# Optimization experiments

Hardware: AMD Instinct MI355X
Metric: run time of the kernel (lower is better)

## Reference

```python
import jax, jax.numpy as jnp
import numpy as np

N_NODES = 100000
N_EDGES = 600000
D = 128          # embedding_dim == hidden_dim
OUT = 128        # output_dim
L = 5            # number of GINConv layers


def setup_inputs() -> dict:
    key = jax.random.key(0)
    ks = jax.random.split(key, 9)
    return {
        "x": jax.random.randint(ks[0], (N_NODES,), 0, N_NODES),
        "edge_index": jax.random.randint(ks[1], (2, N_EDGES), 0, N_NODES),
        "emb": jax.random.normal(ks[2], (N_NODES, D), dtype=jnp.float32) * 0.02,
        "Wa": jax.random.normal(ks[3], (L, D, D), dtype=jnp.float32) * 0.05,
        "ba": jnp.zeros((L, D), dtype=jnp.float32),
        "Wb": jax.random.normal(ks[4], (L, D, D), dtype=jnp.float32) * 0.05,
        "bb": jnp.zeros((L, D), dtype=jnp.float32),
        "Wlin": jax.random.normal(ks[5], (D, OUT), dtype=jnp.float32) * 0.05,
        "blin": jnp.zeros((OUT,), dtype=jnp.float32),
    }


def reference(x, edge_index, emb, Wa, ba, Wb, bb, Wlin, blin):
    src, dst = edge_index[0], edge_index[1]
    h = emb[x]  # [N, D] embedding lookup
    for l in range(L):
        # GINConv with eps=0: mlp((1+eps)*x_i + sum_{j->i} x_j)
        agg = jax.ops.segment_sum(h[src], dst, num_segments=N_NODES)  # [N, D]
        z = h + agg
        z = jax.nn.relu(z @ Wa[l] + ba[l])  # MLP hidden
        z = z @ Wb[l] + bb[l]               # MLP out
        h = jax.nn.relu(z)                  # outer F.relu in forward
    pooled = jnp.sum(h, axis=0, keepdims=True)  # global_add_pool, batch=None -> [1, D]
    return pooled @ Wlin + blin                  # [1, OUT]
```

## Files before the change

### kernel.cpp

```cpp
#include <hip/hip_runtime.h>

#define D 128
#define NLAYERS 5

using short8  = __attribute__((ext_vector_type(8))) short;
using short4v = __attribute__((ext_vector_type(4))) short;
using floatx4 = __attribute__((ext_vector_type(4))) float;
using floatx2 = __attribute__((ext_vector_type(2))) float;

__device__ __forceinline__ unsigned bf16_rne(float x) {
    unsigned u = __float_as_uint(x);
    return (u + 0x7fffu + ((u >> 16) & 1u)) >> 16;
}
__device__ __forceinline__ float bf16_to_f32(short s) {
    return __uint_as_float(((unsigned)(unsigned short)s) << 16);
}

#define HSCALE 16.0f
#define HSCALE_INV 0.0625f

__global__ void prepA_kernel(const int* __restrict__ x, const float* __restrict__ emb,
                             const float* __restrict__ Wa, const float* __restrict__ Wb,
                             const int* __restrict__ edst,
                             unsigned char* __restrict__ H0, short* __restrict__ wt,
                             int* __restrict__ deg,
                             int n_nodes, int n_edges) {
    const int gtid = blockIdx.x * 256 + threadIdx.x;
    const int gsz  = gridDim.x * 256;
    for (int g = gtid; g < 2 * NLAYERS * D * D; g += gsz) {
        int mat = g >> 14, idx = g & 16383;
        int n = idx >> 7, k = idx & 127;
        const float* W = (mat & 1) ? (Wb + (size_t)(mat >> 1) * D * D)
                                   : (Wa + (size_t)(mat >> 1) * D * D);
        wt[g] = (short)bf16_rne(W[k * D + n]);
    }
    for (int t = gtid; t < n_nodes * 32; t += gsz) {
        int node = t >> 5, lane = t & 31;
        int s = x[node];
        const float4 v = *reinterpret_cast<const float4*>(emb + (size_t)s * D + lane * 4);
        int w = __builtin_amdgcn_cvt_pk_fp8_f32(v.x * HSCALE, v.y * HSCALE, 0, false);
        w = __builtin_amdgcn_cvt_pk_fp8_f32(v.z * HSCALE, v.w * HSCALE, w, true);
        reinterpret_cast<unsigned int*>(H0)[(size_t)node * 32 + lane] = (unsigned int)w;
    }
    for (int e = gtid; e < n_edges; e += gsz) atomicAdd(&deg[edst[e]], 1);
}

#define SCAN_TILE 1024
__global__ void scan_sums_kernel(const int* __restrict__ deg, int* __restrict__ bsums, int n) {
    __shared__ int red[256];
    int base = blockIdx.x * SCAN_TILE + threadIdx.x * 4;
    int s = 0;
    #pragma unroll
    for (int j = 0; j < 4; j++) {
        int i = base + j;
        if (i < n) s += deg[i];
    }
    red[threadIdx.x] = s;
    __syncthreads();
    for (int off = 128; off > 0; off >>= 1) {
        if (threadIdx.x < off) red[threadIdx.x] += red[threadIdx.x + off];
        __syncthreads();
    }
    if (threadIdx.x == 0) bsums[blockIdx.x] = red[0];
}

__global__ void scan_bsums_kernel(int* __restrict__ bsums, int nblocks) {
    __shared__ int sdata[256];
    int carry = 0;
    for (int base = 0; base < nblocks; base += 256) {
        int i = base + threadIdx.x;
        int v = (i < nblocks) ? bsums[i] : 0;
        sdata[threadIdx.x] = v;
        __syncthreads();
        for (int off = 1; off < 256; off <<= 1) {
            int t = (threadIdx.x >= off) ? sdata[threadIdx.x - off] : 0;
            __syncthreads();
            sdata[threadIdx.x] += t;
            __syncthreads();
        }
        int incl = sdata[threadIdx.x];
        if (i < nblocks) bsums[i] = carry + incl - v;
        carry += sdata[255];
        __syncthreads();
    }
}

__global__ void scan_final_kernel(const int* __restrict__ deg, const int* __restrict__ bsums,
                                  int* __restrict__ offsets, int* __restrict__ cursor, int n) {
    __shared__ int sdata[256];
    int base = blockIdx.x * SCAN_TILE + threadIdx.x * 4;
    int v[4];
    int s = 0;
    #pragma unroll
    for (int j = 0; j < 4; j++) {
        int i = base + j;
        v[j] = (i < n) ? deg[i] : 0;
        s += v[j];
    }
    sdata[threadIdx.x] = s;
    __syncthreads();
    for (int off = 1; off < 256; off <<= 1) {
        int t = (threadIdx.x >= off) ? sdata[threadIdx.x - off] : 0;
        __syncthreads();
        sdata[threadIdx.x] += t;
        __syncthreads();
    }
    int excl = sdata[threadIdx.x] - s + bsums[blockIdx.x];
    #pragma unroll
    for (int j = 0; j < 4; j++) {
        int i = base + j;
        if (i <= n) offsets[i] = excl;
        if (i < n) cursor[i] = excl;
        excl += v[j];
    }
}

__global__ void fill_kernel(const int* __restrict__ esrc, const int* __restrict__ edst,
                            int* __restrict__ cursor, int* __restrict__ csr_src, int n_edges) {
    int e = blockIdx.x * 256 + threadIdx.x;
    if (e >= n_edges) return;
    int pos = atomicAdd(&cursor[edst[e]], 1);
    csr_src[pos] = esrc[e];
}

__global__ __launch_bounds__(256) void agg_kernel(
        const int* __restrict__ offsets, const int* __restrict__ csr_src,
        const unsigned char* __restrict__ h_in, short* __restrict__ z, int n_rows) {
    const int t   = blockIdx.x * 256 + threadIdx.x;
    const int row = t >> 3;
    const int l8  = t & 7;
    if (row >= n_rows) return;

    float acc[16];
    {
        uint4 w = *reinterpret_cast<const uint4*>(h_in + (size_t)row * D + l8 * 16);
        unsigned int wd[4] = {w.x, w.y, w.z, w.w};
        #pragma unroll
        for (int k = 0; k < 4; k++) {
            floatx2 lo = __builtin_amdgcn_cvt_pk_f32_fp8((int)wd[k], false);
            floatx2 hi = __builtin_amdgcn_cvt_pk_f32_fp8((int)wd[k], true);
            acc[4 * k]     = lo[0]; acc[4 * k + 1] = lo[1];
            acc[4 * k + 2] = hi[0]; acc[4 * k + 3] = hi[1];
        }
    }
    int e   = offsets[row];
    int end = offsets[row + 1];
    for (; e + 3 < end; e += 4) {
        int sA = csr_src[e];
        int sB = csr_src[e + 1];
        int sC = csr_src[e + 2];
        int sD = csr_src[e + 3];
        uint4 wA = *reinterpret_cast<const uint4*>(h_in + (size_t)sA * D + l8 * 16);
        uint4 wB = *reinterpret_cast<const uint4*>(h_in + (size_t)sB * D + l8 * 16);
        uint4 wC = *reinterpret_cast<const uint4*>(h_in + (size_t)sC * D + l8 * 16);
        uint4 wD = *reinterpret_cast<const uint4*>(h_in + (size_t)sD * D + l8 * 16);
        unsigned int da[4] = {wA.x, wA.y, wA.z, wA.w};
        unsigned int db[4] = {wB.x, wB.y, wB.z, wB.w};
        unsigned int dc[4] = {wC.x, wC.y, wC.z, wC.w};
        unsigned int dd[4] = {wD.x, wD.y, wD.z, wD.w};
        #pragma unroll
        for (int k = 0; k < 4; k++) {
            floatx2 alo = __builtin_amdgcn_cvt_pk_f32_fp8((int)da[k], false);
            floatx2 ahi = __builtin_amdgcn_cvt_pk_f32_fp8((int)da[k], true);
            floatx2 blo = __builtin_amdgcn_cvt_pk_f32_fp8((int)db[k], false);
            floatx2 bhi = __builtin_amdgcn_cvt_pk_f32_fp8((int)db[k], true);
            floatx2 clo = __builtin_amdgcn_cvt_pk_f32_fp8((int)dc[k], false);
            floatx2 chi = __builtin_amdgcn_cvt_pk_f32_fp8((int)dc[k], true);
            floatx2 dlo = __builtin_amdgcn_cvt_pk_f32_fp8((int)dd[k], false);
            floatx2 dhi = __builtin_amdgcn_cvt_pk_f32_fp8((int)dd[k], true);
            acc[4 * k]     += (alo[0] + blo[0]) + (clo[0] + dlo[0]);
            acc[4 * k + 1] += (alo[1] + blo[1]) + (clo[1] + dlo[1]);
            acc[4 * k + 2] += (ahi[0] + bhi[0]) + (chi[0] + dhi[0]);
            acc[4 * k + 3] += (ahi[1] + bhi[1]) + (chi[1] + dhi[1]);
        }
    }
    for (; e < end; e++) {
        int sA = csr_src[e];
        uint4 wA = *reinterpret_cast<const uint4*>(h_in + (size_t)sA * D + l8 * 16);
        unsigned int da[4] = {wA.x, wA.y, wA.z, wA.w};
        #pragma unroll
        for (int k = 0; k < 4; k++) {
            floatx2 alo = __builtin_amdgcn_cvt_pk_f32_fp8((int)da[k], false);
            floatx2 ahi = __builtin_amdgcn_cvt_pk_f32_fp8((int)da[k], true);
            acc[4 * k]     += alo[0];
            acc[4 * k + 1] += alo[1];
            acc[4 * k + 2] += ahi[0];
            acc[4 * k + 3] += ahi[1];
        }
    }
    short8 o0, o1;
    #pragma unroll
    for (int j = 0; j < 8; j++) {
        o0[j] = (short)bf16_rne(acc[j] * HSCALE_INV);
        o1[j] = (short)bf16_rne(acc[8 + j] * HSCALE_INV);
    }
    *reinterpret_cast<short8*>(z + (size_t)row * D + l8 * 16)     = o0;
    *reinterpret_cast<short8*>(z + (size_t)row * D + l8 * 16 + 8) = o1;
}

__global__ __launch_bounds__(256, 2) void mlp_kernel(
        const short* __restrict__ z, const short* __restrict__ wta,
        const short* __restrict__ wtb, const float* __restrict__ ba,
        const float* __restrict__ bb, unsigned char* __restrict__ h_out,
        float* __restrict__ pooled_accum, int n_rows, int n_tiles) {
    __shared__ __align__(16) short wash[128 * 128];
    __shared__ __align__(16) short wbsh[128 * 128];
    __shared__ __align__(16) short tsh[4][16 * 128];

    const int tid = threadIdx.x;

    #pragma unroll
    for (int i = 0; i < 8; i++) {
        int g = i * 256 + tid;
        int n = g >> 4, c = g & 15;
        int off = (n * 16 + (c ^ (n & 15))) * 8;
        *reinterpret_cast<short8*>(&wash[off]) =
            *reinterpret_cast<const short8*>(wta + n * D + c * 8);
        *reinterpret_cast<short8*>(&wbsh[off]) =
            *reinterpret_cast<const short8*>(wtb + n * D + c * 8);
    }
    __syncthreads();

    const int lane = tid & 63;
    const int wv   = tid >> 6;
    const int lm   = lane & 15;
    const int quad = lane >> 4;
    short* myt = &tsh[wv][0];

    float bva[8], bvb[8];
    #pragma unroll
    for (int cs = 0; cs < 8; cs++) {
        bva[cs] = ba[cs * 16 + lm];
        bvb[cs] = bb[cs * 16 + lm];
    }

    float poolsum[8];
    #pragma unroll
    for (int cs = 0; cs < 8; cs++) poolsum[cs] = 0.f;

    const int wave_id = blockIdx.x * 4 + wv;
    const int n_waves = gridDim.x * 4;

    for (int tile = wave_id; tile < n_tiles; tile += n_waves) {
        const int row0 = tile * 16;
        const int r    = row0 + lm;

        short8 av[4];
        #pragma unroll
        for (int ks = 0; ks < 4; ks++) {
            if (r < n_rows)
                av[ks] = *reinterpret_cast<const short8*>(z + (size_t)r * D + (ks * 4 + quad) * 8);
            else
                av[ks] = short8{0, 0, 0, 0, 0, 0, 0, 0};
        }

        floatx4 acc1[8];
        #pragma unroll
        for (int cs = 0; cs < 8; cs++) acc1[cs] = floatx4{0.f, 0.f, 0.f, 0.f};
        #pragma unroll
        for (int ks = 0; ks < 4; ks++) {
            const int c = ks * 4 + quad;
            #pragma unroll
            for (int cs = 0; cs < 8; cs++) {
                int nn = cs * 16 + lm;
                short8 bv = *reinterpret_cast<const short8*>(&wash[(nn * 16 + (c ^ (nn & 15))) * 8]);
                acc1[cs] = __builtin_amdgcn_mfma_f32_16x16x32_bf16(av[ks], bv, acc1[cs], 0, 0, 0);
            }
        }

        #pragma unroll
        for (int cs = 0; cs < 8; cs++) {
            int col = cs * 16 + lm;
            int cj = col >> 3, ci = col & 7;
            #pragma unroll
            for (int reg = 0; reg < 4; reg++) {
                int tr = quad * 4 + reg;
                float v = fmaxf(acc1[cs][reg] + bva[cs], 0.f);
                myt[(tr * 16 + (cj ^ tr)) * 8 + ci] = (short)bf16_rne(v);
            }
        }

        short8 av2[4];
        #pragma unroll
        for (int ks = 0; ks < 4; ks++) {
            const int c = ks * 4 + quad;
            av2[ks] = *reinterpret_cast<const short8*>(&myt[(lm * 16 + (c ^ lm)) * 8]);
        }

        floatx4 acc2[8];
        #pragma unroll
        for (int cs = 0; cs < 8; cs++) acc2[cs] = floatx4{0.f, 0.f, 0.f, 0.f};
        #pragma unroll
        for (int ks = 0; ks < 4; ks++) {
            const int c = ks * 4 + quad;
            #pragma unroll
            for (int cs = 0; cs < 8; cs++) {
                int nn = cs * 16 + lm;
                short8 bv = *reinterpret_cast<const short8*>(&wbsh[(nn * 16 + (c ^ (nn & 15))) * 8]);
                acc2[cs] = __builtin_amdgcn_mfma_f32_16x16x32_bf16(av2[ks], bv, acc2[cs], 0, 0, 0);
            }
        }

        #pragma unroll
        for (int cs = 0; cs < 8; cs++) {
            int col = cs * 16 + lm;
            #pragma unroll
            for (int reg = 0; reg < 4; reg++) {
                int rr = row0 + quad * 4 + reg;
                if (rr < n_rows) {
                    float v = fmaxf(acc2[cs][reg] + bvb[cs], 0.f);
                    if (h_out != nullptr) {
                        float sv = v * HSCALE;
                        int pw = __builtin_amdgcn_cvt_pk_fp8_f32(sv, sv, 0, false);
                        h_out[(size_t)rr * D + col] = (unsigned char)(pw & 0xff);
                    }
                    poolsum[cs] += v;
                }
            }
        }
    }

    if (pooled_accum != nullptr) {
        #pragma unroll
        for (int cs = 0; cs < 8; cs++) {
            float v = poolsum[cs];
            v += __shfl_xor(v, 16);
            v += __shfl_xor(v, 32);
            if (quad == 0) atomicAdd(&pooled_accum[cs * 16 + lm], v);
        }
    }
}

__global__ void final_kernel(const float* __restrict__ pooled, const float* __restrict__ Wlin,
                             const float* __restrict__ blin, float* __restrict__ out) {
    const int j = threadIdx.x;
    __shared__ float p[D];
    p[j] = pooled[j];
    __syncthreads();
    float s = blin[j];
    #pragma unroll 8
    for (int k = 0; k < D; k++) s += p[k] * Wlin[k * D + j];
    out[j] = s;
}

extern "C" void kernel_launch(void* const* d_in, const int* in_sizes, int n_in,
                              void* d_out, int out_size, void* d_ws, size_t ws_size,
                              hipStream_t stream) {
    const int*   x    = (const int*)d_in[0];
    const int*   ei   = (const int*)d_in[1];
    const float* emb  = (const float*)d_in[2];
    const float* Wa   = (const float*)d_in[3];
    const float* ba   = (const float*)d_in[4];
    const float* Wb   = (const float*)d_in[5];
    const float* bb   = (const float*)d_in[6];
    const float* Wlin = (const float*)d_in[7];
    const float* blin = (const float*)d_in[8];
    float* out = (float*)d_out;

    const int N = in_sizes[0];
    const int E = in_sizes[1] / 2;
    const int* esrc = ei;
    const int* edst = ei + E;

    unsigned char* H0 = (unsigned char*)d_ws;
    unsigned char* H1 = H0 + (size_t)N * D;
    short* zbuf = (short*)(H1 + (size_t)N * D);
    float* pooled = (float*)(zbuf + (size_t)N * D);
    int* deg     = (int*)(pooled + 128);
    int* offsets = deg + N;
    int* cursor  = offsets + (N + 1);
    int* bsums   = cursor + N;
    int* csr_src = bsums + 4096;
    uintptr_t wt_addr = ((uintptr_t)(csr_src + E) + 15) & ~(uintptr_t)15;
    short* wt = (short*)wt_addr;

    const int scan_blocks = (N + 1 + SCAN_TILE - 1) / SCAN_TILE;

    hipMemsetAsync(pooled, 0, (size_t)(128 + N) * sizeof(int), stream);

    prepA_kernel<<<1024, 256, 0, stream>>>(x, emb, Wa, Wb, edst, H0, wt, deg, N, E);
    scan_sums_kernel<<<scan_blocks, 256, 0, stream>>>(deg, bsums, N);
    scan_bsums_kernel<<<1, 256, 0, stream>>>(bsums, scan_blocks);
    scan_final_kernel<<<scan_blocks, 256, 0, stream>>>(deg, bsums, offsets, cursor, N);
    fill_kernel<<<(E + 255) / 256, 256, 0, stream>>>(esrc, edst, cursor, csr_src, E);

    const int agg_blocks = (N * 8 + 255) / 256;
    const int n_tiles    = (N + 15) / 16;
    unsigned char* hin = H0; unsigned char* hout = H1;
    for (int l = 0; l < NLAYERS; l++) {
        const bool last = (l == NLAYERS - 1);
        float* pacc = last ? pooled : nullptr;
        unsigned char* hdst = last ? nullptr : hout;
        agg_kernel<<<agg_blocks, 256, 0, stream>>>(offsets, csr_src, hin, zbuf, N);
        mlp_kernel<<<512, 256, 0, stream>>>(
            zbuf, wt + (size_t)(2 * l) * D * D, wt + (size_t)(2 * l + 1) * D * D,
            ba + (size_t)l * D, bb + (size_t)l * D, hdst, pacc, N, n_tiles);
        unsigned char* tmp = hin; hin = hout; hout = tmp;
    }

    final_kernel<<<1, 128, 0, stream>>>(pooled, Wlin, blin, out);
}
```

Before: 415.1 us.

## Split fused MLP into two GEMM kernels reading weights from global memory

Replaces the fused two-layer MLP kernel, which staged both weight matrices in LDS, with two separate kernels. Each kernel reads its weights directly from global/L2 into registers, and the first writes its ReLU output back over zbuf in place. The goal is to drop the large LDS footprint and per-block weight staging so occupancy can rise (launch bounds go to 4 blocks per SM, 1024 blocks). The cost is an extra round trip of the hidden activation through global memory, one more launch per layer, and weight reloads per tile from cache.

```diff
diff --git a/kernel.cpp b/kernel.cpp
--- a/kernel.cpp
+++ b/kernel.cpp
@@ -198,135 +198,148 @@
     *reinterpret_cast<short8*>(z + (size_t)row * D + l8 * 16 + 8) = o1;
 }
 
-__global__ __launch_bounds__(256, 2) void mlp_kernel(
-        const short* __restrict__ z, const short* __restrict__ wta,
-        const short* __restrict__ wtb, const float* __restrict__ ba,
-        const float* __restrict__ bb, unsigned char* __restrict__ h_out,
-        float* __restrict__ pooled_accum, int n_rows, int n_tiles) {
-    __shared__ __align__(16) short wash[128 * 128];
-    __shared__ __align__(16) short wbsh[128 * 128];
-    __shared__ __align__(16) short tsh[4][16 * 128];
-
-    const int tid = threadIdx.x;
-
-    #pragma unroll
-    for (int i = 0; i < 8; i++) {
-        int g = i * 256 + tid;
-        int n = g >> 4, c = g & 15;
-        int off = (n * 16 + (c ^ (n & 15))) * 8;
-        *reinterpret_cast<short8*>(&wash[off]) =
-            *reinterpret_cast<const short8*>(wta + n * D + c * 8);
-        *reinterpret_cast<short8*>(&wbsh[off]) =
-            *reinterpret_cast<const short8*>(wtb + n * D + c * 8);
-    }
-    __syncthreads();
-
+__global__ __launch_bounds__(256, 4) void gemm1_kernel(
+        short* __restrict__ zt, const short* __restrict__ wta,
+        const float* __restrict__ ba, int n_rows, int n_tiles) {
+    const int tid  = threadIdx.x;
     const int lane = tid & 63;
     const int wv   = tid >> 6;
     const int lm   = lane & 15;
     const int quad = lane >> 4;
-    short* myt = &tsh[wv][0];
-
-    float bva[8], bvb[8];
-    #pragma unroll
-    for (int cs = 0; cs < 8; cs++) {
-        bva[cs] = ba[cs * 16 + lm];
-        bvb[cs] = bb[cs * 16 + lm];
-    }
-
-    float poolsum[8];
-    #pragma unroll
-    for (int cs = 0; cs < 8; cs++) poolsum[cs] = 0.f;
+
+    float bva[8];
+    #pragma unroll
+    for (int j = 0; j < 8; j++) bva[j] = ba[j * 16 + lm];
 
     const int wave_id = blockIdx.x * 4 + wv;
     const int n_waves = gridDim.x * 4;
-
     for (int tile = wave_id; tile < n_tiles; tile += n_waves) {
         const int row0 = tile * 16;
         const int r    = row0 + lm;
-
         short8 av[4];
         #pragma unroll
         for (int ks = 0; ks < 4; ks++) {
             if (r < n_rows)
-                av[ks] = *reinterpret_cast<const short8*>(z + (size_t)r * D + (ks * 4 + quad) * 8);
+                av[ks] = *reinterpret_cast<const short8*>(zt + (size_t)r * D + (ks * 4 + quad) * 8);
             else
                 av[ks] = short8{0, 0, 0, 0, 0, 0, 0, 0};
         }
-
-        floatx4 acc1[8];
-        #pragma unroll
-        for (int cs = 0; cs < 8; cs++) acc1[cs] = floatx4{0.f, 0.f, 0.f, 0.f};
-        #pragma unroll
-        for (int ks = 0; ks < 4; ks++) {
-            const int c = ks * 4 + quad;
-            #pragma unroll
-            for (int cs = 0; cs < 8; cs++) {
-                int nn = cs * 16 + lm;
-                short8 bv = *reinterpret_cast<const short8*>(&wash[(nn * 16 + (c ^ (nn & 15))) * 8]);
-                acc1[cs] = __builtin_amdgcn_mfma_f32_16x16x32_bf16(av[ks], bv, acc1[cs], 0, 0, 0);
-            }
-        }
-
-        #pragma unroll
-        for (int cs = 0; cs < 8; cs++) {
-            int col = cs * 16 + lm;
-            int cj = col >> 3, ci = col & 7;
-            #pragma unroll
-            for (int reg = 0; reg < 4; reg++) {
-                int tr = quad * 4 + reg;
-                float v = fmaxf(acc1[cs][reg] + bva[cs], 0.f);
-                myt[(tr * 16 + (cj ^ tr)) * 8 + ci] = (short)bf16_rne(v);
-            }
-        }
-
-        short8 av2[4];
-        #pragma unroll
-        for (int ks = 0; ks < 4; ks++) {
-            const int c = ks * 4 + quad;
-            av2[ks] = *reinterpret_cast<const short8*>(&myt[(lm * 16 + (c ^ lm)) * 8]);
-        }
-
-        floatx4 acc2[8];
-        #pragma unroll
-        for (int cs = 0; cs < 8; cs++) acc2[cs] = floatx4{0.f, 0.f, 0.f, 0.f};
-        #pragma unroll
-        for (int ks = 0; ks < 4; ks++) {
-            const int c = ks * 4 + quad;
-            #pragma unroll
-            for (int cs = 0; cs < 8; cs++) {
-                int nn = cs * 16 + lm;
-                short8 bv = *reinterpret_cast<const short8*>(&wbsh[(nn * 16 + (c ^ (nn & 15))) * 8]);
-                acc2[cs] = __builtin_amdgcn_mfma_f32_16x16x32_bf16(av2[ks], bv, acc2[cs], 0, 0, 0);
-            }
-        }
-
-        #pragma unroll
-        for (int cs = 0; cs < 8; cs++) {
-            int col = cs * 16 + lm;
-            #pragma unroll
-            for (int reg = 0; reg < 4; reg++) {
-                int rr = row0 + quad * 4 + reg;
-                if (rr < n_rows) {
-                    float v = fmaxf(acc2[cs][reg] + bvb[cs], 0.f);
-                    if (h_out != nullptr) {
-                        float sv = v * HSCALE;
-                        int pw = __builtin_amdgcn_cvt_pk_fp8_f32(sv, sv, 0, false);
-                        h_out[(size_t)rr * D + col] = (unsigned char)(pw & 0xff);
-                    }
-                    poolsum[cs] += v;
+        const short* wp = wta;
+        asm volatile("" : "+s"(wp));
+        #pragma unroll
+        for (int h = 0; h < 2; h++) {
+            short8 bw[4][4];
+            #pragma unroll
+            for (int ks = 0; ks < 4; ks++)
+                #pragma unroll
+                for (int cs = 0; cs < 4; cs++) {
+                    int nn = h * 64 + cs * 16 + lm;
+                    bw[ks][cs] = *reinterpret_cast<const short8*>(
+                        wp + (size_t)nn * D + (ks * 4 + quad) * 8);
+                }
+            floatx4 acc[4];
+            #pragma unroll
+            for (int cs = 0; cs < 4; cs++) acc[cs] = floatx4{0.f, 0.f, 0.f, 0.f};
+            #pragma unroll
+            for (int ks = 0; ks < 4; ks++)
+                #pragma unroll
+                for (int cs = 0; cs < 4; cs++)
+                    acc[cs] = __builtin_amdgcn_mfma_f32_16x16x32_bf16(av[ks], bw[ks][cs], acc[cs], 0, 0, 0);
+            #pragma unroll
+            for (int cs = 0; cs < 4; cs++) {
+                int col = h * 64 + cs * 16 + lm;
+                float bv = bva[h * 4 + cs];
+                #pragma unroll
+                for (int reg = 0; reg < 4; reg++) {
+                    int rr = row0 + quad * 4 + reg;
+                    if (rr < n_rows)
+                        zt[(size_t)rr * D + col] = (short)bf16_rne(fmaxf(acc[cs][reg] + bv, 0.f));
                 }
             }
         }
     }
+}
+
+__global__ __launch_bounds__(256, 4) void gemm2_kernel(
+        const short* __restrict__ t, const short* __restrict__ wtb,
+        const float* __restrict__ bb, unsigned char* __restrict__ h_out,
+        float* __restrict__ pooled_accum, int n_rows, int n_tiles) {
+    const int tid  = threadIdx.x;
+    const int lane = tid & 63;
+    const int wv   = tid >> 6;
+    const int lm   = lane & 15;
+    const int quad = lane >> 4;
+
+    float bvb[8];
+    #pragma unroll
+    for (int j = 0; j < 8; j++) bvb[j] = bb[j * 16 + lm];
+
+    float poolsum[8];
+    #pragma unroll
+    for (int j = 0; j < 8; j++) poolsum[j] = 0.f;
+
+    const int wave_id = blockIdx.x * 4 + wv;
+    const int n_waves = gridDim.x * 4;
+    for (int tile = wave_id; tile < n_tiles; tile += n_waves) {
+        const int row0 = tile * 16;
+        const int r    = row0 + lm;
+        short8 av[4];
+        #pragma unroll
+        for (int ks = 0; ks < 4; ks++) {
+            if (r < n_rows)
+                av[ks] = *reinterpret_cast<const short8*>(t + (size_t)r * D + (ks * 4 + quad) * 8);
+            else
+                av[ks] = short8{0, 0, 0, 0, 0, 0, 0, 0};
+        }
+        const short* wp = wtb;
+        asm volatile("" : "+s"(wp));
+        #pragma unroll
+        for (int h = 0; h < 2; h++) {
+            short8 bw[4][4];
+            #pragma unroll
+            for (int ks = 0; ks < 4; ks++)
+                #pragma unroll
+                for (int cs = 0; cs < 4; cs++) {
+                    int nn = h * 64 + cs * 16 + lm;
+                    bw[ks][cs] = *reinterpret_cast<const short8*>(
+                        wp + (size_t)nn * D + (ks * 4 + quad) * 8);
+                }
+            floatx4 acc[4];
+            #pragma unroll
+            for (int cs = 0; cs < 4; cs++) acc[cs] = floatx4{0.f, 0.f, 0.f, 0.f};
+            #pragma unroll
+            for (int ks = 0; ks < 4; ks++)
+                #pragma unroll
+                for (int cs = 0; cs < 4; cs++)
+                    acc[cs] = __builtin_amdgcn_mfma_f32_16x16x32_bf16(av[ks], bw[ks][cs], acc[cs], 0, 0, 0);
+            #pragma unroll
+            for (int cs = 0; cs < 4; cs++) {
+                int col = h * 64 + cs * 16 + lm;
+                float bv = bvb[h * 4 + cs];
+                #pragma unroll
+                for (int reg = 0; reg < 4; reg++) {
+                    int rr = row0 + quad * 4 + reg;
+                    if (rr < n_rows) {
+                        float v = fmaxf(acc[cs][reg] + bv, 0.f);
+                        if (h_out != nullptr) {
+                            float sv = v * HSCALE;
+                            int pw = __builtin_amdgcn_cvt_pk_fp8_f32(sv, sv, 0, false);
+                            h_out[(size_t)rr * D + col] = (unsigned char)(pw & 0xff);
+                        }
+                        poolsum[h * 4 + cs] += v;
+                    }
+                }
+            }
+        }
+    }
 
     if (pooled_accum != nullptr) {
         #pragma unroll
-        for (int cs = 0; cs < 8; cs++) {
-            float v = poolsum[cs];
+        for (int j = 0; j < 8; j++) {
+            float v = poolsum[j];
             v += __shfl_xor(v, 16);
             v += __shfl_xor(v, 32);
-            if (quad == 0) atomicAdd(&pooled_accum[cs * 16 + lm], v);
+            if (quad == 0) atomicAdd(&pooled_accum[j * 16 + lm], v);
         }
     }
 }
@@ -384,17 +397,19 @@
     scan_final_kernel<<<scan_blocks, 256, 0, stream>>>(deg, bsums, offsets, cursor, N);
     fill_kernel<<<(E + 255) / 256, 256, 0, stream>>>(esrc, edst, cursor, csr_src, E);
 
-    const int agg_blocks = (N * 8 + 255) / 256;
-    const int n_tiles    = (N + 15) / 16;
+    const int agg_blocks  = (N * 8 + 255) / 256;
+    const int n_tiles     = (N + 15) / 16;
+    const int gemm_blocks = 1024;
     unsigned char* hin = H0; unsigned char* hout = H1;
     for (int l = 0; l < NLAYERS; l++) {
         const bool last = (l == NLAYERS - 1);
         float* pacc = last ? pooled : nullptr;
         unsigned char* hdst = last ? nullptr : hout;
         agg_kernel<<<agg_blocks, 256, 0, stream>>>(offsets, csr_src, hin, zbuf, N);
-        mlp_kernel<<<512, 256, 0, stream>>>(
-            zbuf, wt + (size_t)(2 * l) * D * D, wt + (size_t)(2 * l + 1) * D * D,
-            ba + (size_t)l * D, bb + (size_t)l * D, hdst, pacc, N, n_tiles);
+        gemm1_kernel<<<gemm_blocks, 256, 0, stream>>>(
+            zbuf, wt + (size_t)(2 * l) * D * D, ba + (size_t)l * D, N, n_tiles);
+        gemm2_kernel<<<gemm_blocks, 256, 0, stream>>>(
+            zbuf, wt + (size_t)(2 * l + 1) * D * D, bb + (size_t)l * D, hdst, pacc, N, n_tiles);
         unsigned char* tmp = hin; hin = hout; hout = tmp;
     }
 
```

Measured after the change: 708.5 us. 70.7% more time.
